# Performance work log

Hardware: AMD Instinct MI355X
Metric: run time of the kernel (lower is better)

## Reference

```python
import jax, jax.numpy as jnp
import numpy as np

DIM = 512
HID = 1536          # int(2*(4*512)/3) rounded up to multiple of 256
N_EXPERTS = 8
TOP_K = 2
SHARED_HID = HID * 2  # n_shared_experts scales hidden dim of the single shared MLP
B, S = 4, 2048


def _swiglu(x, w1, w3, w2):
    return (jax.nn.silu(x @ w1.T) * (x @ w3.T)) @ w2.T


def setup_inputs() -> dict:
    key = jax.random.key(0)
    ks = jax.random.split(key, 8)
    sc_d = 1.0 / np.sqrt(DIM)
    sc_h = 1.0 / np.sqrt(HID)
    sc_sh = 1.0 / np.sqrt(SHARED_HID)
    return {
        "x": jax.random.normal(ks[0], (B, S, DIM), jnp.float32),
        "gate_w": jax.random.normal(ks[1], (N_EXPERTS, DIM), jnp.float32) * sc_d,
        "w1": jax.random.normal(ks[2], (N_EXPERTS, HID, DIM), jnp.float32) * sc_d,
        "w3": jax.random.normal(ks[3], (N_EXPERTS, HID, DIM), jnp.float32) * sc_d,
        "w2": jax.random.normal(ks[4], (N_EXPERTS, DIM, HID), jnp.float32) * sc_h,
        "sw1": jax.random.normal(ks[5], (SHARED_HID, DIM), jnp.float32) * sc_d,
        "sw3": jax.random.normal(ks[6], (SHARED_HID, DIM), jnp.float32) * sc_d,
        "sw2": jax.random.normal(ks[7], (DIM, SHARED_HID), jnp.float32) * sc_sh,
    }


def reference(x, gate_w, w1, w3, w2, sw1, sw3, sw2):
    b, s, d = x.shape
    t = b * s
    xf = x.reshape(t, d)

    # --- gate (greedy top-k over softmax scores, fp32) ---
    logits = xf.astype(jnp.float32) @ gate_w.astype(jnp.float32).T  # [T, E]
    scores = jax.nn.softmax(logits, axis=-1)
    topk_w, topk_i = jax.lax.top_k(scores, TOP_K)                    # [T, K]

    # per-token combine weight for each expert: sum of topk weights routed to it
    e = gate_w.shape[0]
    comb = jnp.zeros((t, e), jnp.float32).at[jnp.arange(t)[:, None], topk_i].add(topk_w)

    # --- routed experts: weighted sum of SwiGLU outputs ---
    y = jnp.zeros((t, d), x.dtype)
    for i in range(e):  # fixed small number of structurally distinct experts
        ye = _swiglu(xf, w1[i], w3[i], w2[i]).astype(x.dtype)
        y = y + comb[:, i:i + 1].astype(x.dtype) * ye
    y = y.reshape(b, s, d)

    # --- shared expert added to all tokens ---
    shared = _swiglu(xf, sw1, sw3, sw2).reshape(b, s, d).astype(x.dtype)
    return y + shared
```

## Files before the change

### kernel.cpp

```cpp
#include <hip/hip_runtime.h>

#define T_TOK 8192
#define DIMSZ 512
#define HIDSZ 1536
#define SHIDSZ 3072
#define NE 8

typedef __attribute__((ext_vector_type(4))) float f32x4;
typedef __attribute__((ext_vector_type(8))) short s16x8;

#define SBAR() __builtin_amdgcn_s_barrier()

__device__ __forceinline__ unsigned short f2bf(float f) {
  unsigned int u = __float_as_uint(f);
  u += 0x7fff + ((u >> 16) & 1);
  return (unsigned short)(u >> 16);
}

__device__ __forceinline__ void async16(void* lds, const void* g) {
  __builtin_amdgcn_global_load_lds((const __attribute__((address_space(1))) void*)g,
                                   (__attribute__((address_space(3))) void*)lds,
                                   16, 0, 0);
}

__global__ void cvt_bf16(const float* __restrict__ s, unsigned short* __restrict__ d, int n4) {
  int i = blockIdx.x * blockDim.x + threadIdx.x;
  if (i < n4) {
    float4 v = ((const float4*)s)[i];
    ushort4 o;
    o.x = f2bf(v.x); o.y = f2bf(v.y); o.z = f2bf(v.z); o.w = f2bf(v.w);
    ((ushort4*)d)[i] = o;
  }
}

#define GATE_BLOCKS 256
#define GATE_TPB (T_TOK / GATE_BLOCKS)
#define GATE_TPW (GATE_TPB / 4)

__global__ __launch_bounds__(256) void gate_kernel(
    const float* __restrict__ x, const float* __restrict__ gw,
    float* __restrict__ tw, int* __restrict__ ti, int* __restrict__ cnt) {
  __shared__ int lcnt[NE];
  const int tid = threadIdx.x;
  if (tid < NE) lcnt[tid] = 0;
  __syncthreads();
  const int w = tid >> 6, l = tid & 63;

  float gv[NE][8];
  const float* gbase = gw + l * 8;
#pragma unroll
  for (int e = 0; e < NE; ++e)
#pragma unroll
    for (int j = 0; j < 8; ++j) gv[e][j] = gbase[e * DIMSZ + j];

  const int tok0 = blockIdx.x * GATE_TPB + w * GATE_TPW;
  for (int it = 0; it < GATE_TPW; ++it) {
    const int t = tok0 + it;
    const float* xr = x + (size_t)t * DIMSZ + l * 8;
    float xv[8];
#pragma unroll
    for (int j = 0; j < 8; ++j) xv[j] = xr[j];
    float p[NE];
#pragma unroll
    for (int e = 0; e < NE; ++e) {
      float s = 0.f;
#pragma unroll
      for (int j = 0; j < 8; ++j) s = fmaf(xv[j], gv[e][j], s);
      p[e] = s;
    }
#pragma unroll
    for (int e = 0; e < NE; ++e) {
      float v = p[e];
#pragma unroll
      for (int off = 32; off > 0; off >>= 1) v += __shfl_xor(v, off);
      p[e] = v;
    }
    float m = p[0];
#pragma unroll
    for (int e = 1; e < NE; ++e) m = fmaxf(m, p[e]);
    float ex[NE], s = 0.f;
#pragma unroll
    for (int e = 0; e < NE; ++e) { ex[e] = __expf(p[e] - m); s += ex[e]; }
    float inv = 1.f / s;
    int e0 = 0; float v0 = p[0];
#pragma unroll
    for (int e = 1; e < NE; ++e) if (p[e] > v0) { v0 = p[e]; e0 = e; }
    int e1 = -1; float v1 = -3.4e38f;
#pragma unroll
    for (int e = 0; e < NE; ++e) if (e != e0 && p[e] > v1) { v1 = p[e]; e1 = e; }
    if (l == 0) {
      ti[2 * t] = e0;     tw[2 * t] = ex[e0] * inv;
      ti[2 * t + 1] = e1; tw[2 * t + 1] = ex[e1] * inv;
      atomicAdd(&lcnt[e0], 1);
      atomicAdd(&lcnt[e1], 1);
    }
  }
  __syncthreads();
  if (tid < NE) atomicAdd(&cnt[tid], lcnt[tid]);
}

__global__ void scan_kernel(const int* __restrict__ cnt, int* __restrict__ base,
                            int* __restrict__ cursor) {
  if (threadIdx.x == 0 && blockIdx.x == 0) {
    int r = 0;
    for (int e = 0; e < NE; ++e) { base[e] = r; cursor[e] = r; r += cnt[e]; }
  }
}

__global__ __launch_bounds__(256) void scatter_kernel(
    const int* __restrict__ ti, int* __restrict__ cursor,
    int* __restrict__ tok, int* __restrict__ dst) {
  __shared__ int lcnt[NE], gbase[NE];
  const int tid = threadIdx.x;
  if (tid < NE) lcnt[tid] = 0;
  __syncthreads();
  const int t = blockIdx.x * 256 + tid;
  const int e0 = ti[2 * t], e1 = ti[2 * t + 1];
  const int p0 = atomicAdd(&lcnt[e0], 1);
  const int p1 = atomicAdd(&lcnt[e1], 1);
  __syncthreads();
  if (tid < NE) gbase[tid] = atomicAdd(&cursor[tid], lcnt[tid]);
  __syncthreads();
  const int i0 = gbase[e0] + p0, i1 = gbase[e1] + p1;
  tok[i0] = t; dst[i0] = 2 * t;
  tok[i1] = t; dst[i1] = 2 * t + 1;
}

__global__ void gather_kernel(const unsigned short* __restrict__ xb,
                              const int* __restrict__ tok,
                              unsigned short* __restrict__ xg) {
  int i = blockIdx.x * blockDim.x + threadIdx.x;
  int entry = i >> 6, l = i & 63;
  int t = tok[entry];
  ((uint4*)xg)[entry * 64 + l] = ((const uint4*)xb)[t * 64 + l];
}


template <bool ROUTED>
__global__ __launch_bounds__(256, 2) void gemm1_kernel(
    const unsigned short* __restrict__ A0, const unsigned short* __restrict__ W1,
    const unsigned short* __restrict__ W3, unsigned short* __restrict__ G,
    const int* __restrict__ cnt, const int* __restrict__ base,
    int K, int N, int mtPerE) {
  int e, mt, cntE, rowbase;
  if constexpr (ROUTED) {
    e = blockIdx.x / mtPerE; mt = blockIdx.x % mtPerE;
    cntE = cnt[e];
    if (mt * 128 >= cntE) return;
    rowbase = base[e];
  } else {
    e = 0; mt = blockIdx.x; cntE = T_TOK; rowbase = 0;
  }
  const int m0 = mt * 128;
  const int n0 = blockIdx.y * 64;
  const unsigned short* A = A0 + (size_t)rowbase * K;
  const unsigned short* B1 = W1 + (size_t)e * N * K + (size_t)n0 * K;
  const unsigned short* B3 = W3 + (size_t)e * N * K + (size_t)n0 * K;

  __shared__ __align__(16) unsigned short As[2 * 128 * 64];
  __shared__ __align__(16) unsigned short B1s[2 * 64 * 64];
  __shared__ __align__(16) unsigned short B3s[2 * 64 * 64];

  const int tid = threadIdx.x;
  const int w = tid >> 6, lane = tid & 63;
  const int wr = w >> 1, wc = w & 1;
  const int lhi = lane >> 4, llo = lane & 15;

  const unsigned short* aSrc[4];
  int aDst[4];
#pragma unroll
  for (int i = 0; i < 4; ++i) {
    int L = i * 256 + tid, row = L >> 3, c = L & 7, sc = c ^ (row & 7);
    int ar = ROUTED ? min(m0 + row, cntE - 1) : (m0 + row);
    aSrc[i] = A + (size_t)ar * K + sc * 8;
    aDst[i] = (i * 256 + (tid & ~63)) * 8;
  }
  const unsigned short *b1Src[2], *b3Src[2];
  int bDst[2];
#pragma unroll
  for (int i = 0; i < 2; ++i) {
    int L = i * 256 + tid, row = L >> 3, c = L & 7, sc = c ^ (row & 7);
    b1Src[i] = B1 + (size_t)row * K + sc * 8;
    b3Src[i] = B3 + (size_t)row * K + sc * 8;
    bDst[i] = (i * 256 + (tid & ~63)) * 8;
  }

  int aOff[4][2], bOff[2][2];
#pragma unroll
  for (int m = 0; m < 4; ++m) {
    int r = wr * 64 + m * 16 + llo;
#pragma unroll
    for (int s = 0; s < 2; ++s)
      aOff[m][s] = r * 64 + (((lhi + 4 * s) ^ (r & 7)) * 8);
  }
#pragma unroll
  for (int n = 0; n < 2; ++n) {
    int r = wc * 32 + n * 16 + llo;
#pragma unroll
    for (int s = 0; s < 2; ++s)
      bOff[n][s] = r * 64 + (((lhi + 4 * s) ^ (r & 7)) * 8);
  }

  f32x4 acc1[4][2], acc3[4][2];
#pragma unroll
  for (int m = 0; m < 4; ++m)
#pragma unroll
    for (int n = 0; n < 2; ++n) {
      acc1[m][n] = f32x4{0.f, 0.f, 0.f, 0.f};
      acc3[m][n] = f32x4{0.f, 0.f, 0.f, 0.f};
    }

  const int nt = K >> 6;
  int cur = 0;
#pragma unroll
  for (int i = 0; i < 4; ++i) async16(&As[aDst[i]], aSrc[i]);
#pragma unroll
  for (int i = 0; i < 2; ++i) {
    async16(&B1s[bDst[i]], b1Src[i]);
    async16(&B3s[bDst[i]], b3Src[i]);
  }

  for (int t = 0; t < nt; ++t) {
    const bool more = (t + 1) < nt;
    if (more) {
      const int k1 = (t + 1) << 6;
      const int nxtA = (cur ^ 1) * 8192, nxtB = (cur ^ 1) * 4096;
#pragma unroll
      for (int i = 0; i < 4; ++i) async16(&As[nxtA + aDst[i]], aSrc[i] + k1);
#pragma unroll
      for (int i = 0; i < 2; ++i) {
        async16(&B1s[nxtB + bDst[i]], b1Src[i] + k1);
        async16(&B3s[nxtB + bDst[i]], b3Src[i] + k1);
      }
      asm volatile("s_waitcnt vmcnt(8)" ::: "memory");
    } else {
      asm volatile("s_waitcnt vmcnt(0)" ::: "memory");
    }
    SBAR();
    const int cA = cur * 8192, cB = cur * 4096;
#pragma unroll
    for (int s = 0; s < 2; ++s) {
      s16x8 a[4], b1f[2], b3f[2];
#pragma unroll
      for (int m = 0; m < 4; ++m) a[m] = *(const s16x8*)&As[cA + aOff[m][s]];
#pragma unroll
      for (int n = 0; n < 2; ++n) {
        b1f[n] = *(const s16x8*)&B1s[cB + bOff[n][s]];
        b3f[n] = *(const s16x8*)&B3s[cB + bOff[n][s]];
      }
#pragma unroll
      for (int m = 0; m < 4; ++m)
#pragma unroll
        for (int n = 0; n < 2; ++n) {
          acc1[m][n] = __builtin_amdgcn_mfma_f32_16x16x32_bf16(a[m], b1f[n], acc1[m][n], 0, 0, 0);
          acc3[m][n] = __builtin_amdgcn_mfma_f32_16x16x32_bf16(a[m], b3f[n], acc3[m][n], 0, 0, 0);
        }
    }
    if (more) { SBAR(); cur ^= 1; }
  }

  unsigned short* Grow = G + (size_t)rowbase * N;
#pragma unroll
  for (int m = 0; m < 4; ++m)
#pragma unroll
    for (int n = 0; n < 2; ++n)
#pragma unroll
      for (int q = 0; q < 4; ++q) {
        int r = wr * 64 + m * 16 + lhi * 4 + q;
        if (!ROUTED || (m0 + r) < cntE) {
          float h1 = acc1[m][n][q], h3 = acc3[m][n][q];
          float val = (h1 / (1.f + __expf(-h1))) * h3;
          Grow[(size_t)(m0 + r) * N + n0 + wc * 32 + n * 16 + llo] = f2bf(val);
        }
      }
}

template <bool ROUTED>
__global__ __launch_bounds__(256, 3) void gemm2_kernel(
    const unsigned short* __restrict__ A0, const unsigned short* __restrict__ W2,
    float* __restrict__ Out, const int* __restrict__ cnt, const int* __restrict__ base,
    const int* __restrict__ dst, int K, int mtPerE) {
  int e, mt, cntE, rowbase;
  if constexpr (ROUTED) {
    e = blockIdx.x / mtPerE; mt = blockIdx.x % mtPerE;
    cntE = cnt[e];
    if (mt * 64 >= cntE) return;
    rowbase = base[e];
  } else {
    e = 0; mt = blockIdx.x; cntE = T_TOK; rowbase = 0;
  }
  const int m0 = mt * 64;
  const int n0 = blockIdx.y * 128;
  const unsigned short* A = A0 + (size_t)rowbase * K;
  const unsigned short* B = W2 + (size_t)e * DIMSZ * K + (size_t)n0 * K;

  __shared__ __align__(16) unsigned short As[2 * 64 * 64];
  __shared__ __align__(16) unsigned short Bs[2 * 128 * 64];

  const int tid = threadIdx.x;
  const int w = tid >> 6, lane = tid & 63;
  const int wr = w >> 1, wc = w & 1;
  const int lhi = lane >> 4, llo = lane & 15;

  const unsigned short* aSrc[2];
  int aDst[2];
#pragma unroll
  for (int i = 0; i < 2; ++i) {
    int L = i * 256 + tid, row = L >> 3, c = L & 7, sc = c ^ (row & 7);
    int ar = ROUTED ? min(m0 + row, cntE - 1) : (m0 + row);
    aSrc[i] = A + (size_t)ar * K + sc * 8;
    aDst[i] = (i * 256 + (tid & ~63)) * 8;
  }
  const unsigned short* bSrc[4];
  int bDst[4];
#pragma unroll
  for (int i = 0; i < 4; ++i) {
    int L = i * 256 + tid, row = L >> 3, c = L & 7, sc = c ^ (row & 7);
    bSrc[i] = B + (size_t)row * K + sc * 8;
    bDst[i] = (i * 256 + (tid & ~63)) * 8;
  }

  int aOff[2][2], bOff[4][2];
#pragma unroll
  for (int m = 0; m < 2; ++m) {
    int r = wr * 32 + m * 16 + llo;
#pragma unroll
    for (int s = 0; s < 2; ++s)
      aOff[m][s] = r * 64 + (((lhi + 4 * s) ^ (r & 7)) * 8);
  }
#pragma unroll
  for (int n = 0; n < 4; ++n) {
    int r = wc * 64 + n * 16 + llo;
#pragma unroll
    for (int s = 0; s < 2; ++s)
      bOff[n][s] = r * 64 + (((lhi + 4 * s) ^ (r & 7)) * 8);
  }

  f32x4 acc[2][4];
#pragma unroll
  for (int i = 0; i < 2; ++i)
#pragma unroll
    for (int j = 0; j < 4; ++j) acc[i][j] = f32x4{0.f, 0.f, 0.f, 0.f};

  const int nt = K >> 6;
  int cur = 0;
#pragma unroll
  for (int i = 0; i < 2; ++i) async16(&As[aDst[i]], aSrc[i]);
#pragma unroll
  for (int i = 0; i < 4; ++i) async16(&Bs[bDst[i]], bSrc[i]);

  for (int t = 0; t < nt; ++t) {
    const bool more = (t + 1) < nt;
    if (more) {
      const int k1 = (t + 1) << 6;
      const int nxtA = (cur ^ 1) * 4096, nxtB = (cur ^ 1) * 8192;
#pragma unroll
      for (int i = 0; i < 2; ++i) async16(&As[nxtA + aDst[i]], aSrc[i] + k1);
#pragma unroll
      for (int i = 0; i < 4; ++i) async16(&Bs[nxtB + bDst[i]], bSrc[i] + k1);
      asm volatile("s_waitcnt vmcnt(6)" ::: "memory");
    } else {
      asm volatile("s_waitcnt vmcnt(0)" ::: "memory");
    }
    SBAR();
    const int cA = cur * 4096, cB = cur * 8192;
#pragma unroll
    for (int s = 0; s < 2; ++s) {
      s16x8 a[2], b[4];
#pragma unroll
      for (int m = 0; m < 2; ++m) a[m] = *(const s16x8*)&As[cA + aOff[m][s]];
#pragma unroll
      for (int n = 0; n < 4; ++n) b[n] = *(const s16x8*)&Bs[cB + bOff[n][s]];
#pragma unroll
      for (int i = 0; i < 2; ++i)
#pragma unroll
        for (int j = 0; j < 4; ++j)
          acc[i][j] = __builtin_amdgcn_mfma_f32_16x16x32_bf16(a[i], b[j], acc[i][j], 0, 0, 0);
    }
    if (more) { SBAR(); cur ^= 1; }
  }

#pragma unroll
  for (int i = 0; i < 2; ++i)
#pragma unroll
    for (int j = 0; j < 4; ++j)
#pragma unroll
      for (int q = 0; q < 4; ++q) {
        int r = wr * 32 + i * 16 + lhi * 4 + q;
        if (!ROUTED || (m0 + r) < cntE) {
          int orow;
          if constexpr (ROUTED) orow = dst[rowbase + m0 + r];
          else                  orow = m0 + r;
          Out[(size_t)orow * DIMSZ + n0 + wc * 64 + j * 16 + llo] = acc[i][j][q];
        }
      }
}

__global__ void combine_kernel(const float* __restrict__ shbuf, const float* __restrict__ pair,
                               const float* __restrict__ tw, float* __restrict__ out) {
  int i = blockIdx.x * blockDim.x + threadIdx.x;
  int t = i >> 7, c = i & 127;
  float w0 = tw[2 * t], w1 = tw[2 * t + 1];
  float4 a = ((const float4*)shbuf)[i];
  float4 p0 = ((const float4*)pair)[(size_t)(2 * t) * 128 + c];
  float4 p1 = ((const float4*)pair)[(size_t)(2 * t + 1) * 128 + c];
  float4 o;
  o.x = a.x + w0 * p0.x + w1 * p1.x;
  o.y = a.y + w0 * p0.y + w1 * p1.y;
  o.z = a.z + w0 * p0.z + w1 * p1.z;
  o.w = a.w + w0 * p0.w + w1 * p1.w;
  ((float4*)out)[i] = o;
}

extern "C" void kernel_launch(void* const* d_in, const int* in_sizes, int n_in,
                              void* d_out, int out_size, void* d_ws, size_t ws_size,
                              hipStream_t stream) {
  const float* x   = (const float*)d_in[0];
  const float* gw  = (const float*)d_in[1];
  const float* w1  = (const float*)d_in[2];
  const float* w3  = (const float*)d_in[3];
  const float* w2  = (const float*)d_in[4];
  const float* sw1 = (const float*)d_in[5];
  const float* sw3 = (const float*)d_in[6];
  const float* sw2 = (const float*)d_in[7];
  float* out = (float*)d_out;

  char* p = (char*)d_ws;
  auto alloc = [&](size_t bytes) {
    char* r = p;
    p += (bytes + 255) & ~(size_t)255;
    return r;
  };
  unsigned short* xb   = (unsigned short*)alloc((size_t)T_TOK * DIMSZ * 2);
  unsigned short* xg   = (unsigned short*)alloc((size_t)2 * T_TOK * DIMSZ * 2);
  unsigned short* w1b  = (unsigned short*)alloc((size_t)NE * HIDSZ * DIMSZ * 2);
  unsigned short* w3b  = (unsigned short*)alloc((size_t)NE * HIDSZ * DIMSZ * 2);
  unsigned short* w2b  = (unsigned short*)alloc((size_t)NE * DIMSZ * HIDSZ * 2);
  unsigned short* sw1b = (unsigned short*)alloc((size_t)SHIDSZ * DIMSZ * 2);
  unsigned short* sw3b = (unsigned short*)alloc((size_t)SHIDSZ * DIMSZ * 2);
  unsigned short* sw2b = (unsigned short*)alloc((size_t)DIMSZ * SHIDSZ * 2);
  unsigned short* g    = (unsigned short*)alloc((size_t)T_TOK * SHIDSZ * 2);
  float* pairout = (float*)alloc((size_t)2 * T_TOK * DIMSZ * 4);
  float* shbuf   = (float*)alloc((size_t)T_TOK * DIMSZ * 4);
  float* tw = (float*)alloc((size_t)2 * T_TOK * 4);
  int* ti   = (int*)alloc((size_t)2 * T_TOK * 4);
  int* tok  = (int*)alloc((size_t)2 * T_TOK * 4);
  int* dst  = (int*)alloc((size_t)2 * T_TOK * 4);
  int* meta = (int*)alloc(256);
  int* cnt = meta, *cursor = meta + 8, *base = meta + 16;

  auto cvt = [&](const float* s, unsigned short* d, size_t n) {
    int n4 = (int)(n / 4);
    cvt_bf16<<<(n4 + 255) / 256, 256, 0, stream>>>(s, d, n4);
  };
  cvt(x, xb, (size_t)T_TOK * DIMSZ);
  cvt(w1, w1b, (size_t)NE * HIDSZ * DIMSZ);
  cvt(w3, w3b, (size_t)NE * HIDSZ * DIMSZ);
  cvt(w2, w2b, (size_t)NE * DIMSZ * HIDSZ);
  cvt(sw1, sw1b, (size_t)SHIDSZ * DIMSZ);
  cvt(sw3, sw3b, (size_t)SHIDSZ * DIMSZ);
  cvt(sw2, sw2b, (size_t)DIMSZ * SHIDSZ);

  hipMemsetAsync(meta, 0, 64, stream);
  gate_kernel<<<GATE_BLOCKS, 256, 0, stream>>>(x, gw, tw, ti, cnt);
  scan_kernel<<<1, 64, 0, stream>>>(cnt, base, cursor);
  scatter_kernel<<<T_TOK / 256, 256, 0, stream>>>(ti, cursor, tok, dst);
  gather_kernel<<<(2 * T_TOK * 64) / 256, 256, 0, stream>>>(xb, tok, xg);

  gemm1_kernel<false><<<dim3(T_TOK / 128, SHIDSZ / 64), 256, 0, stream>>>(
      xb, sw1b, sw3b, g, nullptr, nullptr, DIMSZ, SHIDSZ, T_TOK / 128);
  gemm2_kernel<false><<<dim3(T_TOK / 64, DIMSZ / 128), 256, 0, stream>>>(
      g, sw2b, shbuf, nullptr, nullptr, nullptr, SHIDSZ, T_TOK / 64);

  gemm1_kernel<true><<<dim3(NE * (T_TOK / 128), HIDSZ / 64), 256, 0, stream>>>(
      xg, w1b, w3b, g, cnt, base, DIMSZ, HIDSZ, T_TOK / 128);
  gemm2_kernel<true><<<dim3(NE * (T_TOK / 64), DIMSZ / 128), 256, 0, stream>>>(
      g, w2b, pairout, cnt, base, dst, HIDSZ, T_TOK / 64);

  combine_kernel<<<(T_TOK * 128) / 256, 256, 0, stream>>>(shbuf, pairout, tw, out);
}
```

Baseline: 500.7 us.

## Merge shared and routed expert GEMMs, fuse gather and combine via atomics

Merges the shared-expert and routed-expert GEMM launches into one up-projection kernel and one down-projection kernel, each covering both kinds of work in a single grid. The gather kernel is removed by reading token rows through the tok index inside the first GEMM. The combine kernel is removed by having the second GEMM atomically add weighted results into a zeroed output. The first GEMM also drops its LDS double buffering in favour of a single buffer with __syncthreads, which raises the occupancy target and lowers LDS use but exposes load latency. Float atomics make the summation order nondeterministic and add contention on output rows.

Result: faster. 429.9 us (-14.1%).

```diff
diff --git a/kernel.cpp b/kernel.cpp
--- a/kernel.cpp
+++ b/kernel.cpp
@@ -8,8 +8,6 @@
 
 typedef __attribute__((ext_vector_type(4))) float f32x4;
 typedef __attribute__((ext_vector_type(8))) short s16x8;
-
-#define SBAR() __builtin_amdgcn_s_barrier()
 
 __device__ __forceinline__ unsigned short f2bf(float f) {
   unsigned int u = __float_as_uint(f);
@@ -126,40 +124,41 @@
   tok[i1] = t; dst[i1] = 2 * t + 1;
 }
 
-__global__ void gather_kernel(const unsigned short* __restrict__ xb,
-                              const int* __restrict__ tok,
-                              unsigned short* __restrict__ xg) {
-  int i = blockIdx.x * blockDim.x + threadIdx.x;
-  int entry = i >> 6, l = i & 63;
-  int t = tok[entry];
-  ((uint4*)xg)[entry * 64 + l] = ((const uint4*)xb)[t * 64 + l];
-}
-
-
-template <bool ROUTED>
-__global__ __launch_bounds__(256, 2) void gemm1_kernel(
-    const unsigned short* __restrict__ A0, const unsigned short* __restrict__ W1,
-    const unsigned short* __restrict__ W3, unsigned short* __restrict__ G,
-    const int* __restrict__ cnt, const int* __restrict__ base,
-    int K, int N, int mtPerE) {
-  int e, mt, cntE, rowbase;
-  if constexpr (ROUTED) {
-    e = blockIdx.x / mtPerE; mt = blockIdx.x % mtPerE;
+__global__ __launch_bounds__(256, 3) void gemm1_all(
+    const unsigned short* __restrict__ xb, const int* __restrict__ tok,
+    const unsigned short* __restrict__ w1b, const unsigned short* __restrict__ w3b,
+    const unsigned short* __restrict__ sw1b, const unsigned short* __restrict__ sw3b,
+    unsigned short* __restrict__ g_rt, unsigned short* __restrict__ g_sh,
+    const int* __restrict__ cnt, const int* __restrict__ base) {
+  const int bx = blockIdx.x;
+  const int e = bx >> 6, mt = bx & 63;
+  const int n0 = blockIdx.y * 64;
+  int cntE, rowbase, N;
+  const unsigned short *B1, *B3;
+  unsigned short* G;
+  bool indirect;
+  if (e < NE) {
+    N = HIDSZ;
+    if (n0 >= HIDSZ) return;
     cntE = cnt[e];
     if (mt * 128 >= cntE) return;
     rowbase = base[e];
+    B1 = w1b + (size_t)e * HIDSZ * DIMSZ + (size_t)n0 * DIMSZ;
+    B3 = w3b + (size_t)e * HIDSZ * DIMSZ + (size_t)n0 * DIMSZ;
+    G = g_rt + (size_t)rowbase * HIDSZ;
+    indirect = true;
   } else {
-    e = 0; mt = blockIdx.x; cntE = T_TOK; rowbase = 0;
+    N = SHIDSZ; cntE = T_TOK; rowbase = 0;
+    B1 = sw1b + (size_t)n0 * DIMSZ;
+    B3 = sw3b + (size_t)n0 * DIMSZ;
+    G = g_sh;
+    indirect = false;
   }
   const int m0 = mt * 128;
-  const int n0 = blockIdx.y * 64;
-  const unsigned short* A = A0 + (size_t)rowbase * K;
-  const unsigned short* B1 = W1 + (size_t)e * N * K + (size_t)n0 * K;
-  const unsigned short* B3 = W3 + (size_t)e * N * K + (size_t)n0 * K;
-
-  __shared__ __align__(16) unsigned short As[2 * 128 * 64];
-  __shared__ __align__(16) unsigned short B1s[2 * 64 * 64];
-  __shared__ __align__(16) unsigned short B3s[2 * 64 * 64];
+
+  __shared__ __align__(16) unsigned short As[128 * 64];
+  __shared__ __align__(16) unsigned short B1s[64 * 64];
+  __shared__ __align__(16) unsigned short B3s[64 * 64];
 
   const int tid = threadIdx.x;
   const int w = tid >> 6, lane = tid & 63;
@@ -171,8 +170,9 @@
 #pragma unroll
   for (int i = 0; i < 4; ++i) {
     int L = i * 256 + tid, row = L >> 3, c = L & 7, sc = c ^ (row & 7);
-    int ar = ROUTED ? min(m0 + row, cntE - 1) : (m0 + row);
-    aSrc[i] = A + (size_t)ar * K + sc * 8;
+    int ar = min(m0 + row, cntE - 1);
+    int rowg = indirect ? tok[rowbase + ar] : ar;
+    aSrc[i] = xb + (size_t)rowg * DIMSZ + sc * 8;
     aDst[i] = (i * 256 + (tid & ~63)) * 8;
   }
   const unsigned short *b1Src[2], *b3Src[2];
@@ -180,8 +180,8 @@
 #pragma unroll
   for (int i = 0; i < 2; ++i) {
     int L = i * 256 + tid, row = L >> 3, c = L & 7, sc = c ^ (row & 7);
-    b1Src[i] = B1 + (size_t)row * K + sc * 8;
-    b3Src[i] = B3 + (size_t)row * K + sc * 8;
+    b1Src[i] = B1 + (size_t)row * DIMSZ + sc * 8;
+    b3Src[i] = B3 + (size_t)row * DIMSZ + sc * 8;
     bDst[i] = (i * 256 + (tid & ~63)) * 8;
   }
 
@@ -210,43 +210,24 @@
       acc3[m][n] = f32x4{0.f, 0.f, 0.f, 0.f};
     }
 
-  const int nt = K >> 6;
-  int cur = 0;
-#pragma unroll
-  for (int i = 0; i < 4; ++i) async16(&As[aDst[i]], aSrc[i]);
-#pragma unroll
-  for (int i = 0; i < 2; ++i) {
-    async16(&B1s[bDst[i]], b1Src[i]);
-    async16(&B3s[bDst[i]], b3Src[i]);
-  }
-
-  for (int t = 0; t < nt; ++t) {
-    const bool more = (t + 1) < nt;
-    if (more) {
-      const int k1 = (t + 1) << 6;
-      const int nxtA = (cur ^ 1) * 8192, nxtB = (cur ^ 1) * 4096;
-#pragma unroll
-      for (int i = 0; i < 4; ++i) async16(&As[nxtA + aDst[i]], aSrc[i] + k1);
-#pragma unroll
-      for (int i = 0; i < 2; ++i) {
-        async16(&B1s[nxtB + bDst[i]], b1Src[i] + k1);
-        async16(&B3s[nxtB + bDst[i]], b3Src[i] + k1);
-      }
-      asm volatile("s_waitcnt vmcnt(8)" ::: "memory");
-    } else {
-      asm volatile("s_waitcnt vmcnt(0)" ::: "memory");
-    }
-    SBAR();
-    const int cA = cur * 8192, cB = cur * 4096;
+  for (int k0 = 0; k0 < DIMSZ; k0 += 64) {
+#pragma unroll
+    for (int i = 0; i < 4; ++i) async16(&As[aDst[i]], aSrc[i] + k0);
+#pragma unroll
+    for (int i = 0; i < 2; ++i) {
+      async16(&B1s[bDst[i]], b1Src[i] + k0);
+      async16(&B3s[bDst[i]], b3Src[i] + k0);
+    }
+    __syncthreads();
 #pragma unroll
     for (int s = 0; s < 2; ++s) {
       s16x8 a[4], b1f[2], b3f[2];
 #pragma unroll
-      for (int m = 0; m < 4; ++m) a[m] = *(const s16x8*)&As[cA + aOff[m][s]];
+      for (int m = 0; m < 4; ++m) a[m] = *(const s16x8*)&As[aOff[m][s]];
 #pragma unroll
       for (int n = 0; n < 2; ++n) {
-        b1f[n] = *(const s16x8*)&B1s[cB + bOff[n][s]];
-        b3f[n] = *(const s16x8*)&B3s[cB + bOff[n][s]];
+        b1f[n] = *(const s16x8*)&B1s[bOff[n][s]];
+        b3f[n] = *(const s16x8*)&B3s[bOff[n][s]];
       }
 #pragma unroll
       for (int m = 0; m < 4; ++m)
@@ -256,10 +237,9 @@
           acc3[m][n] = __builtin_amdgcn_mfma_f32_16x16x32_bf16(a[m], b3f[n], acc3[m][n], 0, 0, 0);
         }
     }
-    if (more) { SBAR(); cur ^= 1; }
-  }
-
-  unsigned short* Grow = G + (size_t)rowbase * N;
+    __syncthreads();
+  }
+
 #pragma unroll
   for (int m = 0; m < 4; ++m)
 #pragma unroll
@@ -267,32 +247,42 @@
 #pragma unroll
       for (int q = 0; q < 4; ++q) {
         int r = wr * 64 + m * 16 + lhi * 4 + q;
-        if (!ROUTED || (m0 + r) < cntE) {
+        if (m0 + r < cntE) {
           float h1 = acc1[m][n][q], h3 = acc3[m][n][q];
           float val = (h1 / (1.f + __expf(-h1))) * h3;
-          Grow[(size_t)(m0 + r) * N + n0 + wc * 32 + n * 16 + llo] = f2bf(val);
+          G[(size_t)(m0 + r) * N + n0 + wc * 32 + n * 16 + llo] = f2bf(val);
         }
       }
 }
 
-template <bool ROUTED>
-__global__ __launch_bounds__(256, 3) void gemm2_kernel(
-    const unsigned short* __restrict__ A0, const unsigned short* __restrict__ W2,
-    float* __restrict__ Out, const int* __restrict__ cnt, const int* __restrict__ base,
-    const int* __restrict__ dst, int K, int mtPerE) {
-  int e, mt, cntE, rowbase;
-  if constexpr (ROUTED) {
-    e = blockIdx.x / mtPerE; mt = blockIdx.x % mtPerE;
+__global__ __launch_bounds__(256, 3) void gemm2_all(
+    const unsigned short* __restrict__ g_rt, const unsigned short* __restrict__ g_sh,
+    const unsigned short* __restrict__ w2b, const unsigned short* __restrict__ sw2b,
+    const int* __restrict__ cnt, const int* __restrict__ base,
+    const int* __restrict__ dst, const float* __restrict__ tw,
+    float* __restrict__ out) {
+  const int bx = blockIdx.x;
+  const int e = bx >> 7, mt = bx & 127;
+  const int n0 = blockIdx.y * 128;
+  int cntE, rowbase, K;
+  const unsigned short *A, *B;
+  bool routed;
+  if (e < NE) {
     cntE = cnt[e];
     if (mt * 64 >= cntE) return;
     rowbase = base[e];
+    A = g_rt + (size_t)rowbase * HIDSZ;
+    B = w2b + (size_t)e * DIMSZ * HIDSZ + (size_t)n0 * HIDSZ;
+    K = HIDSZ;
+    routed = true;
   } else {
-    e = 0; mt = blockIdx.x; cntE = T_TOK; rowbase = 0;
+    cntE = T_TOK; rowbase = 0;
+    A = g_sh;
+    B = sw2b + (size_t)n0 * SHIDSZ;
+    K = SHIDSZ;
+    routed = false;
   }
   const int m0 = mt * 64;
-  const int n0 = blockIdx.y * 128;
-  const unsigned short* A = A0 + (size_t)rowbase * K;
-  const unsigned short* B = W2 + (size_t)e * DIMSZ * K + (size_t)n0 * K;
 
   __shared__ __align__(16) unsigned short As[2 * 64 * 64];
   __shared__ __align__(16) unsigned short Bs[2 * 128 * 64];
@@ -307,7 +297,7 @@
 #pragma unroll
   for (int i = 0; i < 2; ++i) {
     int L = i * 256 + tid, row = L >> 3, c = L & 7, sc = c ^ (row & 7);
-    int ar = ROUTED ? min(m0 + row, cntE - 1) : (m0 + row);
+    int ar = min(m0 + row, cntE - 1);
     aSrc[i] = A + (size_t)ar * K + sc * 8;
     aDst[i] = (i * 256 + (tid & ~63)) * 8;
   }
@@ -362,7 +352,7 @@
     } else {
       asm volatile("s_waitcnt vmcnt(0)" ::: "memory");
     }
-    SBAR();
+    __builtin_amdgcn_s_barrier();
     const int cA = cur * 4096, cB = cur * 8192;
 #pragma unroll
     for (int s = 0; s < 2; ++s) {
@@ -377,39 +367,30 @@
         for (int j = 0; j < 4; ++j)
           acc[i][j] = __builtin_amdgcn_mfma_f32_16x16x32_bf16(a[i], b[j], acc[i][j], 0, 0, 0);
     }
-    if (more) { SBAR(); cur ^= 1; }
+    if (more) { __builtin_amdgcn_s_barrier(); cur ^= 1; }
   }
 
 #pragma unroll
   for (int i = 0; i < 2; ++i)
 #pragma unroll
-    for (int j = 0; j < 4; ++j)
-#pragma unroll
-      for (int q = 0; q < 4; ++q) {
-        int r = wr * 32 + i * 16 + lhi * 4 + q;
-        if (!ROUTED || (m0 + r) < cntE) {
-          int orow;
-          if constexpr (ROUTED) orow = dst[rowbase + m0 + r];
-          else                  orow = m0 + r;
-          Out[(size_t)orow * DIMSZ + n0 + wc * 64 + j * 16 + llo] = acc[i][j][q];
+    for (int q = 0; q < 4; ++q) {
+      int r = wr * 32 + i * 16 + lhi * 4 + q;
+      if (m0 + r < cntE) {
+        int orow; float wgt;
+        if (routed) {
+          int d = dst[rowbase + m0 + r];
+          orow = d >> 1;
+          wgt = tw[d];
+        } else {
+          orow = m0 + r;
+          wgt = 1.f;
         }
+        float* orow_p = out + (size_t)orow * DIMSZ + n0 + wc * 64 + llo;
+#pragma unroll
+        for (int j = 0; j < 4; ++j)
+          atomicAdd(&orow_p[j * 16], wgt * acc[i][j][q]);
       }
-}
-
-__global__ void combine_kernel(const float* __restrict__ shbuf, const float* __restrict__ pair,
-                               const float* __restrict__ tw, float* __restrict__ out) {
-  int i = blockIdx.x * blockDim.x + threadIdx.x;
-  int t = i >> 7, c = i & 127;
-  float w0 = tw[2 * t], w1 = tw[2 * t + 1];
-  float4 a = ((const float4*)shbuf)[i];
-  float4 p0 = ((const float4*)pair)[(size_t)(2 * t) * 128 + c];
-  float4 p1 = ((const float4*)pair)[(size_t)(2 * t + 1) * 128 + c];
-  float4 o;
-  o.x = a.x + w0 * p0.x + w1 * p1.x;
-  o.y = a.y + w0 * p0.y + w1 * p1.y;
-  o.z = a.z + w0 * p0.z + w1 * p1.z;
-  o.w = a.w + w0 * p0.w + w1 * p1.w;
-  ((float4*)out)[i] = o;
+    }
 }
 
 extern "C" void kernel_launch(void* const* d_in, const int* in_sizes, int n_in,
@@ -432,16 +413,14 @@
     return r;
   };
   unsigned short* xb   = (unsigned short*)alloc((size_t)T_TOK * DIMSZ * 2);
-  unsigned short* xg   = (unsigned short*)alloc((size_t)2 * T_TOK * DIMSZ * 2);
   unsigned short* w1b  = (unsigned short*)alloc((size_t)NE * HIDSZ * DIMSZ * 2);
   unsigned short* w3b  = (unsigned short*)alloc((size_t)NE * HIDSZ * DIMSZ * 2);
   unsigned short* w2b  = (unsigned short*)alloc((size_t)NE * DIMSZ * HIDSZ * 2);
   unsigned short* sw1b = (unsigned short*)alloc((size_t)SHIDSZ * DIMSZ * 2);
   unsigned short* sw3b = (unsigned short*)alloc((size_t)SHIDSZ * DIMSZ * 2);
   unsigned short* sw2b = (unsigned short*)alloc((size_t)DIMSZ * SHIDSZ * 2);
-  unsigned short* g    = (unsigned short*)alloc((size_t)T_TOK * SHIDSZ * 2);
-  float* pairout = (float*)alloc((size_t)2 * T_TOK * DIMSZ * 4);
-  float* shbuf   = (float*)alloc((size_t)T_TOK * DIMSZ * 4);
+  unsigned short* g_rt = (unsigned short*)alloc((size_t)2 * T_TOK * HIDSZ * 2);
+  unsigned short* g_sh = (unsigned short*)alloc((size_t)T_TOK * SHIDSZ * 2);
   float* tw = (float*)alloc((size_t)2 * T_TOK * 4);
   int* ti   = (int*)alloc((size_t)2 * T_TOK * 4);
   int* tok  = (int*)alloc((size_t)2 * T_TOK * 4);
@@ -462,20 +441,14 @@
   cvt(sw2, sw2b, (size_t)DIMSZ * SHIDSZ);
 
   hipMemsetAsync(meta, 0, 64, stream);
+  hipMemsetAsync(out, 0, (size_t)T_TOK * DIMSZ * 4, stream);
   gate_kernel<<<GATE_BLOCKS, 256, 0, stream>>>(x, gw, tw, ti, cnt);
   scan_kernel<<<1, 64, 0, stream>>>(cnt, base, cursor);
   scatter_kernel<<<T_TOK / 256, 256, 0, stream>>>(ti, cursor, tok, dst);
-  gather_kernel<<<(2 * T_TOK * 64) / 256, 256, 0, stream>>>(xb, tok, xg);
-
-  gemm1_kernel<false><<<dim3(T_TOK / 128, SHIDSZ / 64), 256, 0, stream>>>(
-      xb, sw1b, sw3b, g, nullptr, nullptr, DIMSZ, SHIDSZ, T_TOK / 128);
-  gemm2_kernel<false><<<dim3(T_TOK / 64, DIMSZ / 128), 256, 0, stream>>>(
-      g, sw2b, shbuf, nullptr, nullptr, nullptr, SHIDSZ, T_TOK / 64);
-
-  gemm1_kernel<true><<<dim3(NE * (T_TOK / 128), HIDSZ / 64), 256, 0, stream>>>(
-      xg, w1b, w3b, g, cnt, base, DIMSZ, HIDSZ, T_TOK / 128);
-  gemm2_kernel<true><<<dim3(NE * (T_TOK / 64), DIMSZ / 128), 256, 0, stream>>>(
-      g, w2b, pairout, cnt, base, dst, HIDSZ, T_TOK / 64);
-
-  combine_kernel<<<(T_TOK * 128) / 256, 256, 0, stream>>>(shbuf, pairout, tw, out);
-}
+
+  gemm1_all<<<dim3((NE + 1) * (T_TOK / 128), SHIDSZ / 64), 256, 0, stream>>>(
+      xb, tok, w1b, w3b, sw1b, sw3b, g_rt, g_sh, cnt, base);
+
+  gemm2_all<<<dim3(NE * (T_TOK / 64) + (T_TOK / 64), DIMSZ / 128), 256, 0, stream>>>(
+      g_rt, g_sh, w2b, sw2b, cnt, base, dst, tw, out);
+}
```
